# Optimization experiments

Hardware: AMD Instinct MI355X
Metric: run time of the kernel (lower is better)

## Reference

```python
import jax, jax.numpy as jnp
import numpy as np

H = 1024      # hidden_size
I = 2048      # intermediate_size
E = 32        # num_routed_experts
B, S = 4, 2048


def setup_inputs() -> dict:
    key = jax.random.key(0)
    ks = jax.random.split(key, 8)
    scale = 0.02
    inp = {
        "hidden_states": jax.random.normal(ks[0], (B, S, H), dtype=jnp.float32),
        # router gate: stored [H, E] so logits = x @ gate_w
        "gate_w": jax.random.normal(ks[1], (H, E), dtype=jnp.float32) * scale,
        # shared SwiGLU (num_shared_experts=1), weights stored [in, out]
        "shared_gate_w": jax.random.normal(ks[2], (H, I), dtype=jnp.float32) * scale,
        "shared_up_w": jax.random.normal(ks[3], (H, I), dtype=jnp.float32) * scale,
        "shared_down_w": jax.random.normal(ks[4], (I, H), dtype=jnp.float32) * scale,
        # routed grouped SwiGLU, weights stored [E, in, out] (matches GroupedLinear)
        "routed_gate_w": jax.random.normal(ks[5], (E, H, I), dtype=jnp.float32) * scale,
        "routed_up_w": jax.random.normal(ks[6], (E, H, I), dtype=jnp.float32) * scale,
        "routed_down_w": jax.random.normal(ks[7], (E, I, H), dtype=jnp.float32) * scale,
    }
    return inp


def _grouped_mm(a, w, group_sizes):
    # a: [T, in], w: [E, in, out], group_sizes: [E] int32 -> [T, out]
    return jax.lax.ragged_dot(a, w, group_sizes)


def _swiglu(x, gw, uw, dw):
    return (jax.nn.silu(x @ gw) * (x @ uw)) @ dw


def reference(hidden_states, gate_w, shared_gate_w, shared_up_w, shared_down_w,
              routed_gate_w, routed_up_w, routed_down_w):
    b, s, h = hidden_states.shape
    x = hidden_states.reshape(-1, h)                      # [T, H]

    # ---- shared expert ----
    shared_out = _swiglu(x, shared_gate_w, shared_up_w, shared_down_w)

    # ---- router: top-1 ----
    logits = x @ gate_w                                   # [T, E]
    topk_ids = jnp.argmax(logits, axis=-1)                # [T]
    topk_val = jnp.max(logits, axis=-1)                   # [T]
    scores = jax.nn.sigmoid(topk_val)[:, None]            # [T, 1]
    xs = x * scores                                       # scale tokens by router score

    # ---- dispatch: sort tokens by expert id ----
    tokens_per_expert = jnp.zeros((E,), jnp.int32).at[topk_ids].add(1)
    order = jnp.argsort(topk_ids)                         # token ids sorted by expert
    sorted_x = xs[order]                                  # [T, H]

    # ---- grouped SwiGLU experts ----
    g = _grouped_mm(sorted_x, routed_gate_w, tokens_per_expert)   # [T, I]
    u = _grouped_mm(sorted_x, routed_up_w, tokens_per_expert)     # [T, I]
    d = _grouped_mm(jax.nn.silu(g) * u, routed_down_w, tokens_per_expert)  # [T, H]

    # ---- combine: unsort back to token order ----
    inv = jnp.argsort(order)
    routed_out = d[inv]

    return (shared_out + routed_out).reshape(b, s, h)
```

## Files before the change

### kernel.cpp

```cpp
#include <hip/hip_runtime.h>
#include <stdint.h>
#include <stddef.h>

#define TOK 8192
#define H 1024
#define IDIM 2048
#define NE 32
#define BM 128
#define BK 64
#define MAX_TILES 96
#define GUTILES (TOK / BM + MAX_TILES)
#define DNCONV_TILES 16896

typedef __attribute__((ext_vector_type(8))) short short8;
typedef __attribute__((ext_vector_type(4))) float f32x4;
typedef __attribute__((ext_vector_type(4))) float float4v;
typedef __attribute__((ext_vector_type(4))) unsigned int uint4v;


__device__ __forceinline__ unsigned short f2bf(float x) {
  unsigned u = __builtin_bit_cast(unsigned, x);
  u += 0x7fffu + ((u >> 16) & 1u);
  return (unsigned short)(u >> 16);
}

__device__ __forceinline__ unsigned cvtpk(float lo, float hi) {
  unsigned r;
  asm("v_cvt_pk_bf16_f32 %0, %1, %2" : "=v"(r) : "v"(lo), "v"(hi));
  return r;
}

__device__ __forceinline__ void gll16(const void* g, void* l) {
  __builtin_amdgcn_global_load_lds(
      (const __attribute__((address_space(1))) unsigned int*)g,
      (__attribute__((address_space(3))) unsigned int*)l, 16, 0, 0);
}

__device__ __forceinline__ f32x4 mfma16(short8 a, short8 b, f32x4 c) {
  return __builtin_amdgcn_mfma_f32_16x16x32_bf16(a, b, c, 0, 0, 0);
}

__device__ __forceinline__ void tconv_tile(
    const float* __restrict__ src, unsigned short* __restrict__ dst,
    int K, int N, int k0, int n0, int tid, void* smem)
{
  float (*t)[65] = (float(*)[65])smem;
  {
    const int r = tid >> 4;
    const int c = (tid & 15) * 4;
    #pragma unroll
    for (int i = 0; i < 4; ++i) {
      float4v v = *(const float4v*)(src + (size_t)(k0 + r + i * 16) * N + (n0 + c));
      t[r + i * 16][c + 0] = v[0];
      t[r + i * 16][c + 1] = v[1];
      t[r + i * 16][c + 2] = v[2];
      t[r + i * 16][c + 3] = v[3];
    }
  }
  __syncthreads();
  {
    const int n = tid >> 2;
    const int kc = (tid & 3) * 16;
    uint4v o0, o1;
    #pragma unroll
    for (int q = 0; q < 4; ++q) {
      o0[q] = cvtpk(t[kc + 2 * q][n],     t[kc + 2 * q + 1][n]);
      o1[q] = cvtpk(t[kc + 8 + 2 * q][n], t[kc + 8 + 2 * q + 1][n]);
    }
    unsigned short* dp = dst + (size_t)(n0 + n) * K + (k0 + kc);
    *(uint4v*)dp = o0;
    *(uint4v*)(dp + 8) = o1;
  }
}


__global__ __launch_bounds__(256) void tconv_kernel(
    const float* __restrict__ src0, unsigned short* __restrict__ dst0,
    int K, int N)
{
  __shared__ float t[64][65];
  const size_t mat = (size_t)K * N;
  tconv_tile(src0 + (size_t)blockIdx.z * mat, dst0 + (size_t)blockIdx.z * mat,
             K, N, blockIdx.x * 64, blockIdx.y * 64, threadIdx.x, t);
}


__global__ __launch_bounds__(256) void router_kernel(
    const float* __restrict__ x, const float* __restrict__ gw,
    unsigned short* __restrict__ xbf, unsigned short* __restrict__ xsbf,
    int* __restrict__ expert_id, int* __restrict__ counts)
{
  __shared__ float xl[8 * H];
  __shared__ float plog[8][8][NE];
  __shared__ float sscore[8];
  const int tid = threadIdx.x;
  const long t0 = (long)blockIdx.x * 8;

  const float4v* src = (const float4v*)(x + t0 * H);
  float4v* dst = (float4v*)xl;
  #pragma unroll
  for (int i = 0; i < 8; ++i) dst[tid + i * 256] = src[tid + i * 256];
  __syncthreads();

  {
    const int e = tid & 31, c = tid >> 5;
    float acc[8] = {0, 0, 0, 0, 0, 0, 0, 0};
    const float* gp = gw + (c * 128) * NE + e;
    for (int h = 0; h < 128; ++h) {
      float g = gp[h * NE];
      const float* xr = xl + (c * 128 + h);
      #pragma unroll
      for (int tk = 0; tk < 8; ++tk) acc[tk] += xr[tk * H] * g;
    }
    #pragma unroll
    for (int tk = 0; tk < 8; ++tk) plog[c][tk][e] = acc[tk];
  }
  __syncthreads();
  {
    const int e = tid & 31, tok = tid >> 5;
    float lg = 0.f;
    #pragma unroll
    for (int c = 0; c < 8; ++c) lg += plog[c][tok][e];
    float m = lg; int be = e;
    #pragma unroll
    for (int mask = 16; mask >= 1; mask >>= 1) {
      float om = __shfl_xor(m, mask);
      int   oe = __shfl_xor(be, mask);
      if (om > m || (om == m && oe < be)) { m = om; be = oe; }
    }
    if (e == 0) {
      sscore[tok] = 1.f / (1.f + __expf(-m));
      expert_id[t0 + tok] = be;
      atomicAdd(&counts[be], 1);
    }
  }
  __syncthreads();
  {
    const float sc = sscore[tid >> 5];
    const int base = (tid >> 5) * H + (tid & 31) * 32;
    #pragma unroll
    for (int i = 0; i < 4; ++i) {
      uint4v vx, vs;
      #pragma unroll
      for (int q = 0; q < 4; ++q) {
        const float a = xl[base + i * 8 + 2 * q];
        const float b = xl[base + i * 8 + 2 * q + 1];
        vx[q] = cvtpk(a, b);
        vs[q] = cvtpk(a * sc, b * sc);
      }
      *(uint4v*)(xbf  + t0 * H + base + i * 8) = vx;
      *(uint4v*)(xsbf + t0 * H + base + i * 8) = vs;
    }
  }
}


__global__ void scan_kernel(const int* __restrict__ counts, int* __restrict__ offsets,
                            int* __restrict__ cursor, int* __restrict__ tile_e,
                            int* __restrict__ tile_p, int* __restrict__ n_tiles)
{
  if (threadIdx.x != 0) return;
  int off = 0, nt = 0;
  for (int e = 0; e < NE; ++e) {
    offsets[e] = off; cursor[e] = off;
    int cc = counts[e];
    for (int k = 0; k < cc; k += BM) { tile_e[nt] = e; tile_p[nt] = off + k; ++nt; }
    off += cc;
  }
  offsets[NE] = off;
  n_tiles[0] = nt;
}


__global__ __launch_bounds__(256) void perm_kernel(
    const int* __restrict__ expert_id, int* __restrict__ cursor, int* __restrict__ perm)
{
  int t = blockIdx.x * 256 + threadIdx.x;
  int e = expert_id[t];
  int pos = atomicAdd(&cursor[e], 1);
  perm[pos] = t;
}


__global__ __launch_bounds__(256, 2) void gu_kernel(
    const unsigned short* __restrict__ xbf,
    const unsigned short* __restrict__ xsbf,
    const unsigned short* __restrict__ SG, const unsigned short* __restrict__ SU,
    const unsigned short* __restrict__ RG, const unsigned short* __restrict__ RU,
    unsigned short* __restrict__ act_sh, unsigned short* __restrict__ act_rt,
    const float* __restrict__ SDW, const float* __restrict__ RDW,
    unsigned short* __restrict__ SDT, unsigned short* __restrict__ RDT,
    const int* __restrict__ perm, const int* __restrict__ tile_e,
    const int* __restrict__ tile_p, const int* __restrict__ offsets,
    const int* __restrict__ n_tiles)
{
  __shared__ char smem[49152];

  const int tid = threadIdx.x;
  const int bidy = blockIdx.y;

  if (bidy >= GUTILES) {
    const int flat = (bidy - GUTILES) * (int)gridDim.x + (int)blockIdx.x;
    const float* src;
    unsigned short* dst;
    int rem;
    if (flat < 512 * NE) {
      const int e = flat >> 9;
      rem = flat & 511;
      src = RDW + (size_t)e * IDIM * H;
      dst = RDT + (size_t)e * IDIM * H;
    } else {
      rem = flat - 512 * NE;
      src = SDW;
      dst = SDT;
    }
    tconv_tile(src, dst, IDIM, H, (rem >> 4) * 64, (rem & 15) * 64, tid, smem);
    return;
  }

  short* Al = (short*)smem;
  short* Gl = Al + BM * BK;
  short* Ul = Gl + 128 * BK;

  const int wave = tid >> 6, lane = tid & 63;
  const int wm = wave >> 1, wn = wave & 1;

  const bool routed = bidy >= (TOK / BM);
  int row0, row_end;
  const unsigned short *Gt, *Ut, *A;
  unsigned short* act;
  if (routed) {
    const int tx = bidy - TOK / BM;
    if (tx >= *n_tiles) return;
    const int e = tile_e[tx];
    row0 = tile_p[tx];
    row_end = offsets[e + 1];
    Gt = RG + (size_t)e * H * IDIM;
    Ut = RU + (size_t)e * H * IDIM;
    A = xsbf; act = act_rt;
  } else {
    row0 = bidy * BM; row_end = row0 + BM;
    Gt = SG; Ut = SU;
    A = xbf; act = act_sh;
  }
  const int n0 = blockIdx.x * 128;

  const unsigned short *asrc[4], *gsrc[4], *usrc[4];
  int soff[4];
  #pragma unroll
  for (int i = 0; i < 4; ++i) {
    const int r = wave * 32 + i * 8 + (lane >> 3);
    int p = row0 + r;
    if (routed && p >= row_end) p = row0;
    const int arow = routed ? perm[p] : p;
    const int cb = ((lane & 7) * 16) ^ ((r & 7) << 4);
    asrc[i] = A  + (size_t)arow * H + (cb >> 1);
    gsrc[i] = Gt + (size_t)(n0 + r) * H + (cb >> 1);
    usrc[i] = Ut + (size_t)(n0 + r) * H + (cb >> 1);
    soff[i] = (wave * 32 + i * 8) * BK;
  }

  f32x4 accg[4][4] = {};
  f32x4 accu[4][4] = {};

  #pragma unroll 1
  for (int kt = 0; kt < H / BK; ++kt) {
    __syncthreads();
    #pragma unroll
    for (int i = 0; i < 4; ++i) gll16(asrc[i] + kt * BK, Al + soff[i]);
    #pragma unroll
    for (int i = 0; i < 4; ++i) gll16(gsrc[i] + kt * BK, Gl + soff[i]);
    #pragma unroll
    for (int i = 0; i < 4; ++i) gll16(usrc[i] + kt * BK, Ul + soff[i]);
    __syncthreads();

    #pragma unroll
    for (int kk = 0; kk < 2; ++kk) {
      short8 af[4];
      #pragma unroll
      for (int m = 0; m < 4; ++m) {
        const int r = wm * 64 + m * 16 + (lane & 15);
        const int cb = (kk * 64 + ((lane >> 4) * 16)) ^ ((r & 7) << 4);
        af[m] = *(const short8*)((const char*)Al + r * 128 + cb);
      }
      #pragma unroll
      for (int nf = 0; nf < 4; ++nf) {
        const int n = wn * 64 + nf * 16 + (lane & 15);
        const int cb = (kk * 64 + ((lane >> 4) * 16)) ^ ((n & 7) << 4);
        short8 bg = *(const short8*)((const char*)Gl + n * 128 + cb);
        short8 bu = *(const short8*)((const char*)Ul + n * 128 + cb);
        #pragma unroll
        for (int m = 0; m < 4; ++m) {
          accg[m][nf] = mfma16(af[m], bg, accg[m][nf]);
          accu[m][nf] = mfma16(af[m], bu, accu[m][nf]);
        }
      }
    }
  }

  #pragma unroll
  for (int m = 0; m < 4; ++m)
    #pragma unroll
    for (int nf = 0; nf < 4; ++nf) {
      const int col = n0 + wn * 64 + nf * 16 + (lane & 15);
      #pragma unroll
      for (int j = 0; j < 4; ++j) {
        const int row = row0 + wm * 64 + m * 16 + ((lane >> 4) * 4) + j;
        if (routed && row >= row_end) continue;
        const float g = accg[m][nf][j];
        const float u = accu[m][nf][j];
        const float v = (g / (1.f + __expf(-g))) * u;
        act[(size_t)row * IDIM + col] = f2bf(v);
      }
    }
}


template<bool ROUTED>
__global__ __launch_bounds__(256, 4) void dn_kernel(
    const unsigned short* __restrict__ A,
    const unsigned short* __restrict__ DT,
    float* __restrict__ out,
    const int* __restrict__ perm, const int* __restrict__ tile_e,
    const int* __restrict__ tile_p, const int* __restrict__ offsets,
    const int* __restrict__ n_tiles)
{
  __shared__ short Al[BM * BK];
  __shared__ short Dl[128 * BK];

  const int tid = threadIdx.x;
  const int wave = tid >> 6, lane = tid & 63;
  const int wm = wave >> 1, wn = wave & 1;

  int row0, row_end;
  const unsigned short* Dt;
  if constexpr (ROUTED) {
    if ((int)blockIdx.y >= *n_tiles) return;
    const int e = tile_e[blockIdx.y];
    row0 = tile_p[blockIdx.y];
    row_end = offsets[e + 1];
    Dt = DT + (size_t)e * H * IDIM;
  } else {
    row0 = blockIdx.y * BM; row_end = row0 + BM;
    Dt = DT;
  }
  const int n0 = blockIdx.x * 128;

  const unsigned short *asrc[4], *dsrc[4];
  int soff[4];
  #pragma unroll
  for (int i = 0; i < 4; ++i) {
    const int r = wave * 32 + i * 8 + (lane >> 3);
    int p = row0 + r;
    if (ROUTED && p >= row_end) p = row0;
    const int cb = ((lane & 7) * 16) ^ ((r & 7) << 4);
    asrc[i] = A  + (size_t)p * IDIM + (cb >> 1);
    dsrc[i] = Dt + (size_t)(n0 + r) * IDIM + (cb >> 1);
    soff[i] = (wave * 32 + i * 8) * BK;
  }

  f32x4 acc[4][4] = {};

  #pragma unroll 1
  for (int kt = 0; kt < IDIM / BK; ++kt) {
    __syncthreads();
    #pragma unroll
    for (int i = 0; i < 4; ++i) gll16(asrc[i] + kt * BK, Al + soff[i]);
    #pragma unroll
    for (int i = 0; i < 4; ++i) gll16(dsrc[i] + kt * BK, Dl + soff[i]);
    __syncthreads();

    #pragma unroll
    for (int kk = 0; kk < 2; ++kk) {
      short8 af[4];
      #pragma unroll
      for (int m = 0; m < 4; ++m) {
        const int r = wm * 64 + m * 16 + (lane & 15);
        const int cb = (kk * 64 + ((lane >> 4) * 16)) ^ ((r & 7) << 4);
        af[m] = *(const short8*)((const char*)Al + r * 128 + cb);
      }
      #pragma unroll
      for (int nf = 0; nf < 4; ++nf) {
        const int n = wn * 64 + nf * 16 + (lane & 15);
        const int cb = (kk * 64 + ((lane >> 4) * 16)) ^ ((n & 7) << 4);
        short8 bd = *(const short8*)((const char*)Dl + n * 128 + cb);
        #pragma unroll
        for (int m = 0; m < 4; ++m) acc[m][nf] = mfma16(af[m], bd, acc[m][nf]);
      }
    }
  }

  #pragma unroll
  for (int m = 0; m < 4; ++m)
    #pragma unroll
    for (int nf = 0; nf < 4; ++nf) {
      const int col = n0 + wn * 64 + nf * 16 + (lane & 15);
      #pragma unroll
      for (int j = 0; j < 4; ++j) {
        const int row = row0 + wm * 64 + m * 16 + ((lane >> 4) * 4) + j;
        const float v = acc[m][nf][j];
        if constexpr (ROUTED) {
          if (row < row_end) {
            const int t = perm[row];
            out[(size_t)t * H + col] += v;
          }
        } else {
          out[(size_t)row * H + col] = v;
        }
      }
    }
}


extern "C" void kernel_launch(void* const* d_in, const int* in_sizes, int n_in,
                              void* d_out, int out_size, void* d_ws, size_t ws_size,
                              hipStream_t stream) {
  (void)in_sizes; (void)n_in; (void)out_size; (void)ws_size;
  const float* x      = (const float*)d_in[0];
  const float* gate_w = (const float*)d_in[1];
  const float* sgw    = (const float*)d_in[2];
  const float* suw    = (const float*)d_in[3];
  const float* sdw    = (const float*)d_in[4];
  const float* rgw    = (const float*)d_in[5];
  const float* ruw    = (const float*)d_in[6];
  const float* rdw    = (const float*)d_in[7];
  float* out = (float*)d_out;

  char* ws = (char*)d_ws;
  unsigned short* xbf    = (unsigned short*)(ws + 0);
  unsigned short* xsbf   = (unsigned short*)(ws + 16777216);
  unsigned short* act_sh = (unsigned short*)(ws + 33554432);
  int* perm      = (int*)(ws + 67108864);
  int* expert_id = (int*)(ws + 67141632);
  int* counts    = (int*)(ws + 67174400);
  int* offsets   = (int*)(ws + 67174528);
  int* cursor    = (int*)(ws + 67174784);
  int* tile_e    = (int*)(ws + 67174912);
  int* tile_p    = (int*)(ws + 67175424);
  int* n_tiles   = (int*)(ws + 67175936);
  unsigned short* rgwT   = (unsigned short*)(ws + 68157440);
  unsigned short* ruwT   = (unsigned short*)(ws + 202375168);
  unsigned short* rdwT   = (unsigned short*)(ws + 336592896);
  unsigned short* sgwT   = (unsigned short*)(ws + 470810624);
  unsigned short* suwT   = (unsigned short*)(ws + 475004928);
  unsigned short* sdwT   = (unsigned short*)(ws + 479199232);
  unsigned short* act_rt = (unsigned short*)(ws + 483393536);

  hipMemsetAsync(counts, 0, NE * sizeof(int), stream);

  router_kernel<<<TOK / 8, 256, 0, stream>>>(x, gate_w, xbf, xsbf, expert_id, counts);
  scan_kernel<<<1, 64, 0, stream>>>(counts, offsets, cursor, tile_e, tile_p, n_tiles);
  perm_kernel<<<TOK / 256, 256, 0, stream>>>(expert_id, cursor, perm);

  tconv_kernel<<<dim3(H / 64, IDIM / 64, 1), 256, 0, stream>>>(sgw, sgwT, H, IDIM);
  tconv_kernel<<<dim3(H / 64, IDIM / 64, 1), 256, 0, stream>>>(suw, suwT, H, IDIM);
  tconv_kernel<<<dim3(H / 64, IDIM / 64, NE), 256, 0, stream>>>(rgw, rgwT, H, IDIM);
  tconv_kernel<<<dim3(H / 64, IDIM / 64, NE), 256, 0, stream>>>(ruw, ruwT, H, IDIM);
  gu_kernel<<<dim3(IDIM / 128, GUTILES + DNCONV_TILES / (IDIM / 128)), 256, 0, stream>>>(
      xbf, xsbf, sgwT, suwT, rgwT, ruwT, act_sh, act_rt,
      sdw, rdw, sdwT, rdwT,
      perm, tile_e, tile_p, offsets, n_tiles);

  dn_kernel<false><<<dim3(H / 128, TOK / BM), 256, 0, stream>>>(
      act_sh, sdwT, out, perm, tile_e, tile_p, offsets, n_tiles);
  dn_kernel<true><<<dim3(H / 128, MAX_TILES), 256, 0, stream>>>(
      act_rt, rdwT, out, perm, tile_e, tile_p, offsets, n_tiles);
}
```

Before: 624.0 us.

## Fuse router with weight conversion and merge shared/routed down-projection launches

The router kernel and the four weight transpose-conversion launches are merged into one grid, with extra blocks doing conversion tiles. The shared and routed down-projection kernels become a single launch, so both run concurrently instead of serially. The routed result is written to a separate buffer, and a new combine kernel adds it into the output. This removes launch gaps and tail underutilisation but adds a full extra read/write pass over a 32MB buffer for the combine.

```diff
diff --git a/kernel.cpp b/kernel.cpp
--- a/kernel.cpp
+++ b/kernel.cpp
@@ -11,6 +11,8 @@
 #define MAX_TILES 96
 #define GUTILES (TOK / BM + MAX_TILES)
 #define DNCONV_TILES 16896
+#define RT_BLOCKS (TOK / 8)
+#define GUCONV_TILES 33792
 
 typedef __attribute__((ext_vector_type(8))) short short8;
 typedef __attribute__((ext_vector_type(4))) float f32x4;
@@ -74,27 +76,45 @@
 }
 
 
-__global__ __launch_bounds__(256) void tconv_kernel(
-    const float* __restrict__ src0, unsigned short* __restrict__ dst0,
-    int K, int N)
-{
-  __shared__ float t[64][65];
-  const size_t mat = (size_t)K * N;
-  tconv_tile(src0 + (size_t)blockIdx.z * mat, dst0 + (size_t)blockIdx.z * mat,
-             K, N, blockIdx.x * 64, blockIdx.y * 64, threadIdx.x, t);
-}
-
-
-__global__ __launch_bounds__(256) void router_kernel(
+__global__ __launch_bounds__(256) void router_tconv_kernel(
     const float* __restrict__ x, const float* __restrict__ gw,
     unsigned short* __restrict__ xbf, unsigned short* __restrict__ xsbf,
-    int* __restrict__ expert_id, int* __restrict__ counts)
-{
-  __shared__ float xl[8 * H];
-  __shared__ float plog[8][8][NE];
-  __shared__ float sscore[8];
+    int* __restrict__ expert_id, int* __restrict__ counts,
+    const float* __restrict__ sgw, const float* __restrict__ suw,
+    const float* __restrict__ rgw, const float* __restrict__ ruw,
+    unsigned short* __restrict__ sgwT, unsigned short* __restrict__ suwT,
+    unsigned short* __restrict__ rgwT, unsigned short* __restrict__ ruwT)
+{
+  __shared__ char smem[41088];
   const int tid = threadIdx.x;
-  const long t0 = (long)blockIdx.x * 8;
+  const int b = blockIdx.x;
+
+  if (b >= RT_BLOCKS) {
+    const int flat = b - RT_BLOCKS;
+    const float* src;
+    unsigned short* dst;
+    int rem;
+    if (flat < 512 * NE) {
+      const int e = flat >> 9; rem = flat & 511;
+      src = rgw + (size_t)e * H * IDIM; dst = rgwT + (size_t)e * H * IDIM;
+    } else if (flat < 1024 * NE) {
+      const int e = (flat - 512 * NE) >> 9; rem = flat & 511;
+      src = ruw + (size_t)e * H * IDIM; dst = ruwT + (size_t)e * H * IDIM;
+    } else if (flat < 1024 * NE + 512) {
+      rem = flat - 1024 * NE;
+      src = sgw; dst = sgwT;
+    } else {
+      rem = flat - 1024 * NE - 512;
+      src = suw; dst = suwT;
+    }
+    tconv_tile(src, dst, H, IDIM, (rem >> 5) * 64, (rem & 31) * 64, tid, smem);
+    return;
+  }
+
+  float* xl = (float*)smem;
+  float (*plog)[8][NE] = (float(*)[8][NE])(smem + 32768);
+  float* sscore = (float*)(smem + 40960);
+  const long t0 = (long)b * 8;
 
   const float4v* src = (const float4v*)(x + t0 * H);
   float4v* dst = (float4v*)xl;
@@ -144,9 +164,9 @@
       #pragma unroll
       for (int q = 0; q < 4; ++q) {
         const float a = xl[base + i * 8 + 2 * q];
-        const float b = xl[base + i * 8 + 2 * q + 1];
-        vx[q] = cvtpk(a, b);
-        vs[q] = cvtpk(a * sc, b * sc);
+        const float bq = xl[base + i * 8 + 2 * q + 1];
+        vx[q] = cvtpk(a, bq);
+        vs[q] = cvtpk(a * sc, bq * sc);
       }
       *(uint4v*)(xbf  + t0 * H + base + i * 8) = vx;
       *(uint4v*)(xsbf + t0 * H + base + i * 8) = vs;
@@ -316,11 +336,11 @@
 }
 
 
-template<bool ROUTED>
 __global__ __launch_bounds__(256, 4) void dn_kernel(
-    const unsigned short* __restrict__ A,
-    const unsigned short* __restrict__ DT,
-    float* __restrict__ out,
+    const unsigned short* __restrict__ act_sh,
+    const unsigned short* __restrict__ act_rt,
+    const unsigned short* __restrict__ SD, const unsigned short* __restrict__ RD,
+    float* __restrict__ out, float* __restrict__ out_rt,
     const int* __restrict__ perm, const int* __restrict__ tile_e,
     const int* __restrict__ tile_p, const int* __restrict__ offsets,
     const int* __restrict__ n_tiles)
@@ -332,17 +352,22 @@
   const int wave = tid >> 6, lane = tid & 63;
   const int wm = wave >> 1, wn = wave & 1;
 
+  const int bidy = blockIdx.y;
+  const bool routed = bidy >= (TOK / BM);
   int row0, row_end;
-  const unsigned short* Dt;
-  if constexpr (ROUTED) {
-    if ((int)blockIdx.y >= *n_tiles) return;
-    const int e = tile_e[blockIdx.y];
-    row0 = tile_p[blockIdx.y];
+  const unsigned short *Dt, *A;
+  if (routed) {
+    const int tx = bidy - TOK / BM;
+    if (tx >= *n_tiles) return;
+    const int e = tile_e[tx];
+    row0 = tile_p[tx];
     row_end = offsets[e + 1];
-    Dt = DT + (size_t)e * H * IDIM;
+    Dt = RD + (size_t)e * H * IDIM;
+    A = act_rt;
   } else {
-    row0 = blockIdx.y * BM; row_end = row0 + BM;
-    Dt = DT;
+    row0 = bidy * BM; row_end = row0 + BM;
+    Dt = SD;
+    A = act_sh;
   }
   const int n0 = blockIdx.x * 128;
 
@@ -352,7 +377,7 @@
   for (int i = 0; i < 4; ++i) {
     const int r = wave * 32 + i * 8 + (lane >> 3);
     int p = row0 + r;
-    if (ROUTED && p >= row_end) p = row0;
+    if (routed && p >= row_end) p = row0;
     const int cb = ((lane & 7) * 16) ^ ((r & 7) << 4);
     asrc[i] = A  + (size_t)p * IDIM + (cb >> 1);
     dsrc[i] = Dt + (size_t)(n0 + r) * IDIM + (cb >> 1);
@@ -398,17 +423,27 @@
       #pragma unroll
       for (int j = 0; j < 4; ++j) {
         const int row = row0 + wm * 64 + m * 16 + ((lane >> 4) * 4) + j;
+        if (routed && row >= row_end) continue;
         const float v = acc[m][nf][j];
-        if constexpr (ROUTED) {
-          if (row < row_end) {
-            const int t = perm[row];
-            out[(size_t)t * H + col] += v;
-          }
+        if (routed) {
+          const int t = perm[row];
+          out_rt[(size_t)t * H + col] = v;
         } else {
           out[(size_t)row * H + col] = v;
         }
       }
     }
+}
+
+
+__global__ __launch_bounds__(256) void combine_kernel(
+    float* __restrict__ out, const float* __restrict__ out_rt)
+{
+  const size_t i = ((size_t)blockIdx.x * 256 + threadIdx.x) * 4;
+  float4v a = *(float4v*)(out + i);
+  float4v b = *(const float4v*)(out_rt + i);
+  a[0] += b[0]; a[1] += b[1]; a[2] += b[2]; a[3] += b[3];
+  *(float4v*)(out + i) = a;
 }
 
 
@@ -445,24 +480,23 @@
   unsigned short* suwT   = (unsigned short*)(ws + 475004928);
   unsigned short* sdwT   = (unsigned short*)(ws + 479199232);
   unsigned short* act_rt = (unsigned short*)(ws + 483393536);
+  float*          out_rt = (float*)(ws + 516947968);
 
   hipMemsetAsync(counts, 0, NE * sizeof(int), stream);
 
-  router_kernel<<<TOK / 8, 256, 0, stream>>>(x, gate_w, xbf, xsbf, expert_id, counts);
+  router_tconv_kernel<<<RT_BLOCKS + GUCONV_TILES, 256, 0, stream>>>(
+      x, gate_w, xbf, xsbf, expert_id, counts,
+      sgw, suw, rgw, ruw, sgwT, suwT, rgwT, ruwT);
   scan_kernel<<<1, 64, 0, stream>>>(counts, offsets, cursor, tile_e, tile_p, n_tiles);
   perm_kernel<<<TOK / 256, 256, 0, stream>>>(expert_id, cursor, perm);
 
-  tconv_kernel<<<dim3(H / 64, IDIM / 64, 1), 256, 0, stream>>>(sgw, sgwT, H, IDIM);
-  tconv_kernel<<<dim3(H / 64, IDIM / 64, 1), 256, 0, stream>>>(suw, suwT, H, IDIM);
-  tconv_kernel<<<dim3(H / 64, IDIM / 64, NE), 256, 0, stream>>>(rgw, rgwT, H, IDIM);
-  tconv_kernel<<<dim3(H / 64, IDIM / 64, NE), 256, 0, stream>>>(ruw, ruwT, H, IDIM);
   gu_kernel<<<dim3(IDIM / 128, GUTILES + DNCONV_TILES / (IDIM / 128)), 256, 0, stream>>>(
       xbf, xsbf, sgwT, suwT, rgwT, ruwT, act_sh, act_rt,
       sdw, rdw, sdwT, rdwT,
       perm, tile_e, tile_p, offsets, n_tiles);
 
-  dn_kernel<false><<<dim3(H / 128, TOK / BM), 256, 0, stream>>>(
-      act_sh, sdwT, out, perm, tile_e, tile_p, offsets, n_tiles);
-  dn_kernel<true><<<dim3(H / 128, MAX_TILES), 256, 0, stream>>>(
-      act_rt, rdwT, out, perm, tile_e, tile_p, offsets, n_tiles);
-}
+  dn_kernel<<<dim3(H / 128, TOK / BM + MAX_TILES), 256, 0, stream>>>(
+      act_sh, act_rt, sdwT, rdwT, out, out_rt,
+      perm, tile_e, tile_p, offsets, n_tiles);
+  combine_kernel<<<TOK * H / 1024, 256, 0, stream>>>(out, out_rt);
+}
```

Result: faster. 597.9 us, median of 2 (-4.2%).
